# Optimization experiments

Hardware: AMD Instinct MI355X
Metric: run time of the kernel (lower is better)

The kernel has to match this reference:

```python
import jax, jax.numpy as jnp
import numpy as np

D_E = 100   # entity embedding dim
D_R = 100   # relation embedding dim
RANK = 40   # TR rank
N_ENT = 10000
N_REL = 50
B = 128
EPS = 1e-5  # torch BatchNorm1d default eps


def _bn(x, gamma, beta):
    # BatchNorm1d in training mode: biased batch statistics over the batch dim.
    mu = x.mean(axis=0)
    var = x.var(axis=0)  # ddof=0, matches torch normalization variance
    return gamma * (x - mu) * jax.lax.rsqrt(var + EPS) + beta


def _tr_to_tensor(f0, f1, f2, f3):
    # Tensor-ring reconstruction of W with ring trace; factors are [R, d, R].
    # Pairwise contraction keeps intermediates at [R, d, d, R] (256 MB max).
    A = jnp.einsum('aib,bjc->aijc', f0, f1)   # [R, d_r, d_e, R]
    C = jnp.einsum('ckd,dla->ckla', f2, f3)   # [R, d_e, d_e, R]
    return jnp.einsum('aijc,ckla->ijkl', A, C)  # [d_r, d_e, d_e, d_e]


def setup_inputs() -> dict:
    key = jax.random.key(0)
    ks = jax.random.split(key, 10)
    E_weight = 0.001 * jax.random.normal(ks[0], (N_ENT, D_E), dtype=jnp.float32)
    E_weight = E_weight.at[0].set(0.0)  # padding_idx=0
    R_weight = 0.001 * jax.random.normal(ks[1], (N_REL, D_R), dtype=jnp.float32)
    R_weight = R_weight.at[0].set(0.0)
    f0 = jax.random.normal(ks[2], (RANK, D_R, RANK), dtype=jnp.float32) * 0.05
    f1 = jax.random.normal(ks[3], (RANK, D_E, RANK), dtype=jnp.float32) * 0.05
    f2 = jax.random.normal(ks[4], (RANK, D_E, RANK), dtype=jnp.float32) * 0.05
    f3 = jax.random.normal(ks[5], (RANK, D_E, RANK), dtype=jnp.float32) * 0.05
    bnr_g = jnp.ones((D_R,), jnp.float32); bnr_b = jnp.zeros((D_R,), jnp.float32)
    bne_g = jnp.ones((D_E,), jnp.float32); bne_b = jnp.zeros((D_E,), jnp.float32)
    bnw_g = jnp.ones((D_E,), jnp.float32); bnw_b = jnp.zeros((D_E,), jnp.float32)
    r_idx = jax.random.randint(ks[6], (B,), 0, N_REL)
    e_idx1 = jax.random.randint(ks[7], (B,), 0, N_ENT)
    e_idx2 = jax.random.randint(ks[8], (B,), 0, N_ENT)
    return {
        'E_weight': E_weight, 'R_weight': R_weight,
        'f0': f0, 'f1': f1, 'f2': f2, 'f3': f3,
        'bnr_g': bnr_g, 'bnr_b': bnr_b,
        'bne_g': bne_g, 'bne_b': bne_b,
        'bnw_g': bnw_g, 'bnw_b': bnw_b,
        'r_idx': r_idx, 'e_idx1': e_idx1, 'e_idx2': e_idx2,
        'miss_ent_domain': 2,
    }


def reference(E_weight, R_weight, f0, f1, f2, f3,
              bnr_g, bnr_b, bne_g, bne_b, bnw_g, bnw_b,
              r_idx, e_idx1, e_idx2, miss_ent_domain):
    # Reconstruct the full TR tensor every call, as the module does.
    W = _tr_to_tensor(f0, f1, f2, f3)                  # [d_r, d_e, d_e, d_e]
    r = _bn(R_weight[r_idx], bnr_g, bnr_b)             # [B, d_r]
    W_mat = (r @ W.reshape(D_R, -1)).reshape(-1, D_E, D_E, D_E)  # [B, d_e^3]
    # Dropouts are identity here (deterministic / eval mode).
    e1 = _bn(E_weight[e_idx1], bne_g, bne_b)           # [B, d_e]
    e2 = _bn(E_weight[e_idx2], bne_g, bne_b)           # [B, d_e]
    labs = 'ijk'  # ary = 3
    out_lab = labs[miss_ent_domain - 1]
    eq = f'b{labs},' + ','.join(f'b{l}' for l in labs if l != out_lab) + f'->b{out_lab}'
    W_out = jnp.einsum(eq, W_mat, e1, e2)              # [B, d_e]
    W_out = _bn(W_out, bnw_g, bnw_b)
    scores = W_out @ E_weight.T                        # [B, N_ENT]
    pred = jax.nn.softmax(scores, axis=1)
    return (pred, W)
```

## Files before the change

### kernel.cpp

```cpp
#include <hip/hip_runtime.h>
#include <hip/hip_bf16.h>

#define DE 100
#define RK 40
#define NENT 10000
#define BATCH 128
#define KDIM 1600
#define MN 10000
#define PRED_SIZE (BATCH*NENT)

typedef __bf16 bf16x8 __attribute__((ext_vector_type(8)));
typedef float floatx4 __attribute__((ext_vector_type(4)));

static __device__ __forceinline__ unsigned short f2bf(float f) {
    unsigned int u = __builtin_bit_cast(unsigned int, f);
    unsigned int lsb = (u >> 16) & 1u;
    u += 0x7fffu + lsb;
    return (unsigned short)(u >> 16);
}

__global__ void prep_A_kernel(const float* __restrict__ f0, const float* __restrict__ f1,
                              unsigned short* __restrict__ Abf) {
    const int m = blockIdx.x;
    const int i = m / 100, j = m % 100;
    const int t = threadIdx.x;
    __shared__ __align__(16) float P[KDIM];
    __shared__ __align__(16) float Q[KDIM];
    for (int e = t; e < KDIM; e += 256) {
        const int u = e / 40, v = e % 40;
        P[e] = f0[u*4000 + i*40 + v];
        Q[e] = f1[u*4000 + j*40 + v];
    }
    __syncthreads();
    for (int o = t; o < 400; o += 256) {
        const int x  = o / 10;
        const int z4 = (o % 10) * 4;
        float a0=0.f, a1=0.f, a2=0.f, a3=0.f;
        #pragma unroll
        for (int y = 0; y < 40; ++y) {
            const float s = P[x*40 + y];
            const float4 q = *reinterpret_cast<const float4*>(&Q[y*40 + z4]);
            a0 += s*q.x; a1 += s*q.y; a2 += s*q.z; a3 += s*q.w;
        }
        ushort4 r;
        r.x = f2bf(a0); r.y = f2bf(a1); r.z = f2bf(a2); r.w = f2bf(a3);
        *reinterpret_cast<ushort4*>(&Abf[(size_t)m*KDIM + x*40 + z4]) = r;
    }
}

__global__ void prep_B_kernel(const float* __restrict__ f2, const float* __restrict__ f3,
                              unsigned short* __restrict__ Bbf) {
    const int n = blockIdx.x;
    const int k = n / 100, l = n % 100;
    const int t = threadIdx.x;
    __shared__ __align__(16) float P[KDIM];
    __shared__ __align__(16) float Q[KDIM];
    __shared__ __align__(16) float Rt[KDIM];
    for (int e = t; e < KDIM; e += 256) {
        const int u = e / 40, v = e % 40;
        P[e] = f2[u*4000 + k*40 + v];
        Q[e] = f3[u*4000 + l*40 + v];
    }
    __syncthreads();
    for (int o = t; o < 400; o += 256) {
        const int x  = o / 10;
        const int z4 = (o % 10) * 4;
        float a0=0.f, a1=0.f, a2=0.f, a3=0.f;
        #pragma unroll
        for (int y = 0; y < 40; ++y) {
            const float s = P[x*40 + y];
            const float4 q = *reinterpret_cast<const float4*>(&Q[y*40 + z4]);
            a0 += s*q.x; a1 += s*q.y; a2 += s*q.z; a3 += s*q.w;
        }
        Rt[x*40 + z4 + 0] = a0; Rt[x*40 + z4 + 1] = a1;
        Rt[x*40 + z4 + 2] = a2; Rt[x*40 + z4 + 3] = a3;
    }
    __syncthreads();
    for (int o = t; o < 400; o += 256) {
        const int a  = o / 10;
        const int c4 = (o % 10) * 4;
        ushort4 r;
        r.x = f2bf(Rt[(c4+0)*40 + a]);
        r.y = f2bf(Rt[(c4+1)*40 + a]);
        r.z = f2bf(Rt[(c4+2)*40 + a]);
        r.w = f2bf(Rt[(c4+3)*40 + a]);
        *reinterpret_cast<ushort4*>(&Bbf[(size_t)n*KDIM + a*40 + c4]) = r;
    }
}

typedef __attribute__((address_space(1))) void gvoid;
typedef __attribute__((address_space(3))) void lvoid;
static __device__ __forceinline__ void async_cp16(const void* g, void* l) {
    gvoid* gp = (gvoid*)(unsigned long long)g;
    lvoid* lp = (lvoid*)(unsigned int)(unsigned long long)l;
    __builtin_amdgcn_global_load_lds(gp, lp, 16, 0, 0);
}

#define NKT 25
#define LDS_TILE 16384

__global__ __launch_bounds__(512, 2) void gemm_kernel(const unsigned short* __restrict__ A,
                                                      const unsigned short* __restrict__ Bm,
                                                      float* __restrict__ W) {
    extern __shared__ unsigned short lds[];
    const int t = threadIdx.x;
    const int w = t >> 6, l = t & 63;
    const int wm = w >> 2, wn = w & 3;
    const int quad = l >> 4, lrow = l & 15;
    const int swz = lrow & 7;

    const int orig = blockIdx.x;
    const int sb = (orig & 7) * 200 + (orig >> 3);
    const int by = sb / 40, bx = sb % 40;
    const int m0 = by * 256, n0 = bx * 256;

    const int srow = t >> 3;
    const int schk = (t & 7) ^ (srow & 7);
    int offA[4], offB[4];
    #pragma unroll
    for (int i = 0; i < 4; ++i) {
        int ra = m0 + i*64 + srow; if (ra > MN-1) ra = MN-1;
        int rb = n0 + i*64 + srow; if (rb > MN-1) rb = MN-1;
        offA[i] = ra * KDIM + schk * 8;
        offB[i] = rb * KDIM + schk * 8;
    }
    const int lds_off = t * 8;

    floatx4 acc[8][4] = {};

    #pragma unroll
    for (int i = 0; i < 4; ++i) {
        async_cp16(A  + offA[i], lds + i*4096 + lds_off);
        async_cp16(Bm + offB[i], lds + LDS_TILE + i*4096 + lds_off);
    }

    for (int kt = 0; kt < NKT; ++kt) {
        const int cur = kt & 1;
        const unsigned short* As = lds + cur * (2*LDS_TILE);
        const unsigned short* Bs = As + LDS_TILE;

        if (kt < NKT-1) {
            unsigned short* An = lds + (cur ^ 1) * (2*LDS_TILE);
            unsigned short* Bn = An + LDS_TILE;
            const int koff = (kt + 1) * 64;
            #pragma unroll
            for (int i = 0; i < 4; ++i) {
                async_cp16(A  + offA[i] + koff, An + i*4096 + lds_off);
                async_cp16(Bm + offB[i] + koff, Bn + i*4096 + lds_off);
            }
            asm volatile("s_waitcnt vmcnt(8)" ::: "memory");
        } else {
            asm volatile("s_waitcnt vmcnt(0)" ::: "memory");
        }
        __builtin_amdgcn_s_barrier();
        asm volatile("" ::: "memory");

        bf16x8 b[4][2];
        #pragma unroll
        for (int ni = 0; ni < 4; ++ni) {
            const int row = wn*64 + ni*16 + lrow;
            #pragma unroll
            for (int kk = 0; kk < 2; ++kk) {
                const int ch = ((kk << 2) | quad) ^ swz;
                b[ni][kk] = *reinterpret_cast<const bf16x8*>(&Bs[row*64 + ch*8]);
            }
        }
        #pragma unroll
        for (int mh = 0; mh < 2; ++mh) {
            bf16x8 a[4][2];
            #pragma unroll
            for (int mi2 = 0; mi2 < 4; ++mi2) {
                const int row = wm*128 + mh*64 + mi2*16 + lrow;
                #pragma unroll
                for (int kk = 0; kk < 2; ++kk) {
                    const int ch = ((kk << 2) | quad) ^ swz;
                    a[mi2][kk] = *reinterpret_cast<const bf16x8*>(&As[row*64 + ch*8]);
                }
            }
            __builtin_amdgcn_s_setprio(1);
            #pragma unroll
            for (int mi2 = 0; mi2 < 4; ++mi2) {
                #pragma unroll
                for (int ni = 0; ni < 4; ++ni) {
                    acc[mh*4+mi2][ni] = __builtin_amdgcn_mfma_f32_16x16x32_bf16(
                        a[mi2][0], b[ni][0], acc[mh*4+mi2][ni], 0, 0, 0);
                    acc[mh*4+mi2][ni] = __builtin_amdgcn_mfma_f32_16x16x32_bf16(
                        a[mi2][1], b[ni][1], acc[mh*4+mi2][ni], 0, 0, 0);
                }
            }
            __builtin_amdgcn_s_setprio(0);
        }

        asm volatile("s_waitcnt lgkmcnt(0)" ::: "memory");
        __builtin_amdgcn_s_barrier();
        asm volatile("" ::: "memory");
    }

    #pragma unroll
    for (int mi = 0; mi < 8; ++mi) {
        #pragma unroll
        for (int ni = 0; ni < 4; ++ni) {
            #pragma unroll
            for (int reg = 0; reg < 4; ++reg) {
                const int rg = m0 + wm*128 + mi*16 + quad*4 + reg;
                const int cg = n0 + wn*64 + ni*16 + lrow;
                if (rg < MN && cg < MN)
                    W[(size_t)rg * MN + cg] = acc[mi][ni][reg];
            }
        }
    }
}

__global__ void bn_kernel(const float* __restrict__ src, const int* __restrict__ idx,
                          const float* __restrict__ gamma, const float* __restrict__ beta,
                          float* __restrict__ out) {
    const int f = blockIdx.x;
    const int b = threadIdx.x;
    __shared__ float red[BATCH];
    const int row = idx ? idx[b] : b;
    const float x = src[row*DE + f];
    red[b] = x; __syncthreads();
    for (int s = 64; s > 0; s >>= 1) { if (b < s) red[b] += red[b + s]; __syncthreads(); }
    const float mu = red[0] * (1.0f/BATCH);
    __syncthreads();
    const float d = x - mu;
    red[b] = d * d; __syncthreads();
    for (int s = 64; s > 0; s >>= 1) { if (b < s) red[b] += red[b + s]; __syncthreads(); }
    const float var = red[0] * (1.0f/BATCH);
    out[b*DE + f] = gamma[f] * d / sqrtf(var + 1e-5f) + beta[f];
}

__global__ void proj_kernel(const float* __restrict__ rb, const float* __restrict__ e1b,
                            const float* __restrict__ e2b,
                            const float* __restrict__ f0, const float* __restrict__ f1,
                            const float* __restrict__ f2, const float* __restrict__ f3,
                            float* __restrict__ wraw) {
    const int b = blockIdx.x, t = threadIdx.x;
    __shared__ float rv[DE], e1v[DE], e2v[DE];
    __shared__ float R0[KDIM], E1[KDIM], E2[KDIM], T[KDIM], S[KDIM];
    if (t < DE) { rv[t] = rb[b*DE+t]; e1v[t] = e1b[b*DE+t]; e2v[t] = e2b[b*DE+t]; }
    __syncthreads();
    for (int e = t; e < KDIM; e += 256) {
        const int u = e / 40, v = e % 40;
        const int base = u*4000 + v;
        float aR=0.f, aE1=0.f, aE2=0.f;
        for (int p = 0; p < DE; ++p) {
            aR  += rv[p]  * f0[base + p*40];
            aE1 += e1v[p] * f1[base + p*40];
            aE2 += e2v[p] * f3[base + p*40];
        }
        R0[e] = aR; E1[e] = aE1; E2[e] = aE2;
    }
    __syncthreads();
    for (int e = t; e < KDIM; e += 256) {
        const int a = e / 40, c = e % 40;
        float acc = 0.f;
        #pragma unroll
        for (int y = 0; y < 40; ++y) acc += R0[a*40+y] * E1[y*40+c];
        T[e] = acc;
    }
    __syncthreads();
    for (int e = t; e < KDIM; e += 256) {
        const int c = e / 40, d = e % 40;
        float acc = 0.f;
        #pragma unroll
        for (int y = 0; y < 40; ++y) acc += T[y*40+c] * E2[d*40+y];
        S[e] = acc;
    }
    __syncthreads();
    if (t < DE) {
        float acc = 0.f;
        for (int c = 0; c < 40; ++c) {
            #pragma unroll
            for (int d = 0; d < 40; ++d)
                acc += S[c*40+d] * f2[c*4000 + t*40 + d];
        }
        wraw[b*DE + t] = acc;
    }
}

__global__ void scores_kernel(const float* __restrict__ wbn, const float* __restrict__ E,
                              float* __restrict__ scores) {
    const int bx = blockIdx.x;
    const int b = bx >> 3, chunk = bx & 7;
    const int t = threadIdx.x;
    __shared__ __align__(16) float wsh[DE];
    if (t < DE) wsh[t] = wbn[b*DE + t];
    __syncthreads();
    const float4* wv = reinterpret_cast<const float4*>(wsh);
    const int n_end = (chunk + 1) * 1250;
    for (int n = chunk*1250 + t; n < n_end; n += 256) {
        const float4* er = reinterpret_cast<const float4*>(E + (size_t)n * DE);
        float acc = 0.f;
        #pragma unroll
        for (int q = 0; q < 25; ++q) {
            const float4 e4 = er[q], w4 = wv[q];
            acc += e4.x*w4.x + e4.y*w4.y + e4.z*w4.z + e4.w*w4.w;
        }
        scores[(size_t)b*NENT + n] = acc;
    }
}

__global__ void softmax_reduce_kernel(const float* __restrict__ scores,
                                      float* __restrict__ rmax, float* __restrict__ rsum) {
    const int b = blockIdx.x, t = threadIdx.x;
    __shared__ float red[256];
    const float* s = scores + (size_t)b*NENT;
    float m = -1e30f;
    for (int n = t; n < NENT; n += 256) m = fmaxf(m, s[n]);
    red[t] = m; __syncthreads();
    for (int st = 128; st > 0; st >>= 1) { if (t < st) red[t] = fmaxf(red[t], red[t+st]); __syncthreads(); }
    m = red[0]; __syncthreads();
    float sum = 0.f;
    for (int n = t; n < NENT; n += 256) sum += expf(s[n] - m);
    red[t] = sum; __syncthreads();
    for (int st = 128; st > 0; st >>= 1) { if (t < st) red[t] += red[t+st]; __syncthreads(); }
    if (t == 0) { rmax[b] = m; rsum[b] = red[0]; }
}

__global__ void pred_kernel(float* __restrict__ out, const float* __restrict__ rmax,
                            const float* __restrict__ rsum) {
    const int i = blockIdx.x*256 + threadIdx.x;
    const int b = i / NENT;
    out[i] = expf(out[i] - rmax[b]) / rsum[b];
}

extern "C" void kernel_launch(void* const* d_in, const int* in_sizes, int n_in,
                              void* d_out, int out_size, void* d_ws, size_t ws_size,
                              hipStream_t stream) {
    (void)in_sizes; (void)n_in; (void)out_size; (void)ws_size;
    const float* E    = (const float*)d_in[0];
    const float* Rw   = (const float*)d_in[1];
    const float* f0   = (const float*)d_in[2];
    const float* f1   = (const float*)d_in[3];
    const float* f2   = (const float*)d_in[4];
    const float* f3   = (const float*)d_in[5];
    const float* bnrg = (const float*)d_in[6];
    const float* bnrb = (const float*)d_in[7];
    const float* bneg = (const float*)d_in[8];
    const float* bneb = (const float*)d_in[9];
    const float* bnwg = (const float*)d_in[10];
    const float* bnwb = (const float*)d_in[11];
    const int* r_idx  = (const int*)d_in[12];
    const int* e_idx1 = (const int*)d_in[13];
    const int* e_idx2 = (const int*)d_in[14];

    float* out = (float*)d_out;
    float* Wt  = out + PRED_SIZE;

    char* ws = (char*)d_ws;
    unsigned short* Abf = (unsigned short*)ws;
    unsigned short* Bbf = (unsigned short*)(ws + 32000000);
    float* rbn  = (float*)(ws + 64000000);
    float* e1bn = rbn  + BATCH*DE;
    float* e2bn = e1bn + BATCH*DE;
    float* wraw = e2bn + BATCH*DE;
    float* wbn  = wraw + BATCH*DE;
    float* rmax = wbn  + BATCH*DE;
    float* rsum = rmax + BATCH;

    static bool s_attr = false;
    if (!s_attr) {
        hipFuncSetAttribute((const void*)gemm_kernel,
                            hipFuncAttributeMaxDynamicSharedMemorySize, 131072);
        s_attr = true;
    }

    prep_A_kernel<<<MN, 256, 0, stream>>>(f0, f1, Abf);
    prep_B_kernel<<<MN, 256, 0, stream>>>(f2, f3, Bbf);
    gemm_kernel<<<1600, 512, 131072, stream>>>(Abf, Bbf, Wt);

    bn_kernel<<<DE, BATCH, 0, stream>>>(Rw, r_idx, bnrg, bnrb, rbn);
    bn_kernel<<<DE, BATCH, 0, stream>>>(E, e_idx1, bneg, bneb, e1bn);
    bn_kernel<<<DE, BATCH, 0, stream>>>(E, e_idx2, bneg, bneb, e2bn);
    proj_kernel<<<BATCH, 256, 0, stream>>>(rbn, e1bn, e2bn, f0, f1, f2, f3, wraw);
    bn_kernel<<<DE, BATCH, 0, stream>>>(wraw, nullptr, bnwg, bnwb, wbn);
    scores_kernel<<<BATCH*8, 256, 0, stream>>>(wbn, E, out);
    softmax_reduce_kernel<<<BATCH, 256, 0, stream>>>(out, rmax, rsum);
    pred_kernel<<<PRED_SIZE/256, 256, 0, stream>>>(out, rmax, rsum);
}
```

Before: 1.161 ms.

## Interleave GEMM LDS staging with MFMA sub-phases and split projection kernel

The main GEMM loop is restructured into four sub-phases per K tile, each issuing async global-to-LDS copies between LDS fragment reads and MFMA groups, with A and B staged separately. The goal is to hide load latency better and to keep fewer A fragments live in registers. Separately, the three input BatchNorm launches are merged into one kernel. The per-batch projection is split into a parallel stage1 (480 blocks with factors cached in LDS) and a stage2 that does the small contractions, spreading the serial per-batch work across more blocks. Stage1 reuses the Abf workspace region for its output, which is safe only because the GEMM has already finished on the same stream.

```diff
diff --git a/kernel.cpp b/kernel.cpp
--- a/kernel.cpp
+++ b/kernel.cpp
@@ -97,7 +97,6 @@
 }
 
 #define NKT 25
-#define LDS_TILE 16384
 
 __global__ __launch_bounds__(512, 2) void gemm_kernel(const unsigned short* __restrict__ A,
                                                       const unsigned short* __restrict__ Bm,
@@ -116,85 +115,100 @@
 
     const int srow = t >> 3;
     const int schk = (t & 7) ^ (srow & 7);
-    int offA[4], offB[4];
+    const unsigned short* gA[4];
+    const unsigned short* gB[4];
     #pragma unroll
     for (int i = 0; i < 4; ++i) {
         int ra = m0 + i*64 + srow; if (ra > MN-1) ra = MN-1;
         int rb = n0 + i*64 + srow; if (rb > MN-1) rb = MN-1;
-        offA[i] = ra * KDIM + schk * 8;
-        offB[i] = rb * KDIM + schk * 8;
-    }
-    const int lds_off = t * 8;
+        gA[i] = A  + (size_t)ra*KDIM + schk*8;
+        gB[i] = Bm + (size_t)rb*KDIM + schk*8;
+    }
+    const int ldst = t * 8;
+
+    const int ch0  = (quad ^ swz) * 8;
+    const int ch1  = ch0 ^ 32;
+    const int aRow = (wm*128 + lrow) * 64;
+    const int bRow = (wn*64  + lrow) * 64;
+    const unsigned short* pAk0[2] = { lds +         aRow + ch0, lds + 32768 + aRow + ch0 };
+    const unsigned short* pAk1[2] = { lds +         aRow + ch1, lds + 32768 + aRow + ch1 };
+    const unsigned short* pBk0[2] = { lds + 16384 + bRow + ch0, lds + 49152 + bRow + ch0 };
+    const unsigned short* pBk1[2] = { lds + 16384 + bRow + ch1, lds + 49152 + bRow + ch1 };
 
     floatx4 acc[8][4] = {};
-
-    #pragma unroll
-    for (int i = 0; i < 4; ++i) {
-        async_cp16(A  + offA[i], lds + i*4096 + lds_off);
-        async_cp16(Bm + offB[i], lds + LDS_TILE + i*4096 + lds_off);
-    }
-
-    for (int kt = 0; kt < NKT; ++kt) {
-        const int cur = kt & 1;
-        const unsigned short* As = lds + cur * (2*LDS_TILE);
-        const unsigned short* Bs = As + LDS_TILE;
-
-        if (kt < NKT-1) {
-            unsigned short* An = lds + (cur ^ 1) * (2*LDS_TILE);
-            unsigned short* Bn = An + LDS_TILE;
-            const int koff = (kt + 1) * 64;
-            #pragma unroll
-            for (int i = 0; i < 4; ++i) {
-                async_cp16(A  + offA[i] + koff, An + i*4096 + lds_off);
-                async_cp16(Bm + offB[i] + koff, Bn + i*4096 + lds_off);
-            }
-            asm volatile("s_waitcnt vmcnt(8)" ::: "memory");
-        } else {
-            asm volatile("s_waitcnt vmcnt(0)" ::: "memory");
-        }
-        __builtin_amdgcn_s_barrier();
-        asm volatile("" ::: "memory");
-
-        bf16x8 b[4][2];
-        #pragma unroll
-        for (int ni = 0; ni < 4; ++ni) {
-            const int row = wn*64 + ni*16 + lrow;
-            #pragma unroll
-            for (int kk = 0; kk < 2; ++kk) {
-                const int ch = ((kk << 2) | quad) ^ swz;
-                b[ni][kk] = *reinterpret_cast<const bf16x8*>(&Bs[row*64 + ch*8]);
-            }
-        }
-        #pragma unroll
-        for (int mh = 0; mh < 2; ++mh) {
-            bf16x8 a[4][2];
-            #pragma unroll
-            for (int mi2 = 0; mi2 < 4; ++mi2) {
-                const int row = wm*128 + mh*64 + mi2*16 + lrow;
-                #pragma unroll
-                for (int kk = 0; kk < 2; ++kk) {
-                    const int ch = ((kk << 2) | quad) ^ swz;
-                    a[mi2][kk] = *reinterpret_cast<const bf16x8*>(&As[row*64 + ch*8]);
-                }
-            }
-            __builtin_amdgcn_s_setprio(1);
-            #pragma unroll
-            for (int mi2 = 0; mi2 < 4; ++mi2) {
-                #pragma unroll
-                for (int ni = 0; ni < 4; ++ni) {
-                    acc[mh*4+mi2][ni] = __builtin_amdgcn_mfma_f32_16x16x32_bf16(
-                        a[mi2][0], b[ni][0], acc[mh*4+mi2][ni], 0, 0, 0);
-                    acc[mh*4+mi2][ni] = __builtin_amdgcn_mfma_f32_16x16x32_bf16(
-                        a[mi2][1], b[ni][1], acc[mh*4+mi2][ni], 0, 0, 0);
-                }
-            }
-            __builtin_amdgcn_s_setprio(0);
-        }
-
-        asm volatile("s_waitcnt lgkmcnt(0)" ::: "memory");
-        __builtin_amdgcn_s_barrier();
-        asm volatile("" ::: "memory");
-    }
+    bf16x8 bfr[4][2], afr[2][2];
+    int kA = 64, kB = 128;
+
+#define RD_B(c)  do { _Pragma("unroll") for (int ni = 0; ni < 4; ++ni) {              \
+        bfr[ni][0] = *reinterpret_cast<const bf16x8*>(pBk0[c] + ni*1024);             \
+        bfr[ni][1] = *reinterpret_cast<const bf16x8*>(pBk1[c] + ni*1024); } } while(0)
+
+#define RD_A(c,p) do { _Pragma("unroll") for (int j = 0; j < 2; ++j) {                \
+        afr[j][0] = *reinterpret_cast<const bf16x8*>(pAk0[c] + (2*(p)+j)*1024);       \
+        afr[j][1] = *reinterpret_cast<const bf16x8*>(pAk1[c] + (2*(p)+j)*1024); } } while(0)
+
+#define STG_A(c,i0) do { unsigned short* d = lds + (((c)^1)*32768) + (i0)*4096 + ldst; \
+        async_cp16(gA[(i0)]   + kA, d);                                                \
+        async_cp16(gA[(i0)+1] + kA, d + 4096); } while(0)
+
+#define STG_B(c,i0) do { unsigned short* d = lds + ((c)*32768) + 16384 + (i0)*4096 + ldst; \
+        async_cp16(gB[(i0)]   + kB, d);                                                \
+        async_cp16(gB[(i0)+1] + kB, d + 4096); } while(0)
+
+#define BARO() do { __builtin_amdgcn_s_barrier();                                      \
+        asm volatile("s_waitcnt lgkmcnt(0)" ::: "memory");                             \
+        __builtin_amdgcn_sched_barrier(0); } while(0)
+
+#define MM(p) do { __builtin_amdgcn_s_setprio(1);                                      \
+        _Pragma("unroll") for (int j = 0; j < 2; ++j)                                  \
+        _Pragma("unroll") for (int ni = 0; ni < 4; ++ni) {                             \
+            acc[2*(p)+j][ni] = __builtin_amdgcn_mfma_f32_16x16x32_bf16(                \
+                afr[j][0], bfr[ni][0], acc[2*(p)+j][ni], 0, 0, 0);                     \
+            acc[2*(p)+j][ni] = __builtin_amdgcn_mfma_f32_16x16x32_bf16(                \
+                afr[j][1], bfr[ni][1], acc[2*(p)+j][ni], 0, 0, 0); }                   \
+        __builtin_amdgcn_s_setprio(0); } while(0)
+
+#define VMW(n) asm volatile("s_waitcnt vmcnt(" #n ")" ::: "memory")
+
+#define TILE(c, AOK, BOK, VMT) do {                                                    \
+        RD_B(c); RD_A(c,0); if (AOK) { STG_A(c,0); }                                   \
+        BARO(); MM(0); __builtin_amdgcn_s_barrier();                                   \
+        RD_A(c,1); if (AOK) { STG_A(c,2); }                                            \
+        BARO(); MM(1); __builtin_amdgcn_s_barrier();                                   \
+        RD_A(c,2); if (BOK) { STG_B(c,0); }                                            \
+        BARO(); MM(2); __builtin_amdgcn_s_barrier();                                   \
+        RD_A(c,3); if (BOK) { STG_B(c,2); }                                            \
+        BARO(); MM(3);                                                                 \
+        VMT;                                                                           \
+        __builtin_amdgcn_s_barrier();                                                  \
+    } while (0)
+
+    #pragma unroll
+    for (int i = 0; i < 4; ++i) async_cp16(gA[i],      lds +          i*4096 + ldst);
+    #pragma unroll
+    for (int i = 0; i < 4; ++i) async_cp16(gB[i],      lds + 16384 +  i*4096 + ldst);
+    #pragma unroll
+    for (int i = 0; i < 4; ++i) async_cp16(gB[i] + 64, lds + 49152 +  i*4096 + ldst);
+    VMW(4);
+    __builtin_amdgcn_s_barrier();
+
+    for (int it = 0; it < 12; ++it) {
+        TILE(0, true, true, VMW(4));
+        kA += 64; kB += 64;
+        if (it < 11) { TILE(1, true, true,  VMW(4)); }
+        else         { TILE(1, true, false, VMW(0)); }
+        kA += 64; kB += 64;
+    }
+    TILE(0, false, false, ((void)0));
+
+#undef RD_B
+#undef RD_A
+#undef STG_A
+#undef STG_B
+#undef BARO
+#undef MM
+#undef VMW
+#undef TILE
 
     #pragma unroll
     for (int mi = 0; mi < 8; ++mi) {
@@ -211,14 +225,42 @@
     }
 }
 
-__global__ void bn_kernel(const float* __restrict__ src, const int* __restrict__ idx,
+__global__ void bn3_kernel(const float* __restrict__ E, const float* __restrict__ Rw,
+                           const int* __restrict__ r_idx, const int* __restrict__ e_idx1,
+                           const int* __restrict__ e_idx2,
+                           const float* __restrict__ bnrg, const float* __restrict__ bnrb,
+                           const float* __restrict__ bneg, const float* __restrict__ bneb,
+                           float* __restrict__ rbn, float* __restrict__ e1bn,
+                           float* __restrict__ e2bn) {
+    const int grp = blockIdx.x / DE;
+    const int f   = blockIdx.x % DE;
+    const int b   = threadIdx.x;
+    const float* src  = (grp == 0) ? Rw   : E;
+    const int*   idx  = (grp == 0) ? r_idx : (grp == 1 ? e_idx1 : e_idx2);
+    const float* gam  = (grp == 0) ? bnrg : bneg;
+    const float* bet  = (grp == 0) ? bnrb : bneb;
+    float* out        = (grp == 0) ? rbn  : (grp == 1 ? e1bn : e2bn);
+    __shared__ float red[BATCH];
+    const int row = idx[b];
+    const float x = src[row*DE + f];
+    red[b] = x; __syncthreads();
+    for (int s = 64; s > 0; s >>= 1) { if (b < s) red[b] += red[b + s]; __syncthreads(); }
+    const float mu = red[0] * (1.0f/BATCH);
+    __syncthreads();
+    const float d = x - mu;
+    red[b] = d * d; __syncthreads();
+    for (int s = 64; s > 0; s >>= 1) { if (b < s) red[b] += red[b + s]; __syncthreads(); }
+    const float var = red[0] * (1.0f/BATCH);
+    out[b*DE + f] = gam[f] * d / sqrtf(var + 1e-5f) + bet[f];
+}
+
+__global__ void bn_kernel(const float* __restrict__ src,
                           const float* __restrict__ gamma, const float* __restrict__ beta,
                           float* __restrict__ out) {
     const int f = blockIdx.x;
     const int b = threadIdx.x;
     __shared__ float red[BATCH];
-    const int row = idx ? idx[b] : b;
-    const float x = src[row*DE + f];
+    const float x = src[b*DE + f];
     red[b] = x; __syncthreads();
     for (int s = 64; s > 0; s >>= 1) { if (b < s) red[b] += red[b + s]; __syncthreads(); }
     const float mu = red[0] * (1.0f/BATCH);
@@ -230,27 +272,43 @@
     out[b*DE + f] = gamma[f] * d / sqrtf(var + 1e-5f) + beta[f];
 }
 
-__global__ void proj_kernel(const float* __restrict__ rb, const float* __restrict__ e1b,
+__global__ void proj_stage1(const float* __restrict__ rb, const float* __restrict__ e1b,
                             const float* __restrict__ e2b,
                             const float* __restrict__ f0, const float* __restrict__ f1,
-                            const float* __restrict__ f2, const float* __restrict__ f3,
+                            const float* __restrict__ f3,
+                            float* __restrict__ outg) {
+    const int bi = blockIdx.x;
+    const int fi = bi / 160, rest = bi % 160;
+    const int u = rest / 4, b0 = (rest % 4) * 32;
+    const float* vec = (fi == 0) ? rb : (fi == 1 ? e1b : e2b);
+    const float* fac = (fi == 0) ? f0 : (fi == 1 ? f1 : f3);
+    float* og = outg + (size_t)fi * (BATCH*KDIM);
+    __shared__ __align__(16) float F[4000];
+    __shared__ __align__(16) float V[3200];
+    const int t = threadIdx.x;
+    for (int e = t; e < 4000; e += 256) F[e] = fac[u*4000 + e];
+    for (int e = t; e < 3200; e += 256) V[e] = vec[b0*100 + e];
+    __syncthreads();
+    #pragma unroll
+    for (int it = 0; it < 5; ++it) {
+        const int o = t + it*256;
+        const int bb = o / 40, v = o % 40;
+        const float* Vb = &V[bb*100];
+        float acc = 0.f;
+        #pragma unroll 4
+        for (int p = 0; p < 100; ++p) acc += Vb[p] * F[p*40 + v];
+        og[(size_t)(b0+bb)*KDIM + u*40 + v] = acc;
+    }
+}
+
+__global__ void proj_stage2(const float* __restrict__ Rg, const float* __restrict__ f2,
                             float* __restrict__ wraw) {
     const int b = blockIdx.x, t = threadIdx.x;
-    __shared__ float rv[DE], e1v[DE], e2v[DE];
     __shared__ float R0[KDIM], E1[KDIM], E2[KDIM], T[KDIM], S[KDIM];
-    if (t < DE) { rv[t] = rb[b*DE+t]; e1v[t] = e1b[b*DE+t]; e2v[t] = e2b[b*DE+t]; }
-    __syncthreads();
-    for (int e = t; e < KDIM; e += 256) {
-        const int u = e / 40, v = e % 40;
-        const int base = u*4000 + v;
-        float aR=0.f, aE1=0.f, aE2=0.f;
-        for (int p = 0; p < DE; ++p) {
-            aR  += rv[p]  * f0[base + p*40];
-            aE1 += e1v[p] * f1[base + p*40];
-            aE2 += e2v[p] * f3[base + p*40];
-        }
-        R0[e] = aR; E1[e] = aE1; E2[e] = aE2;
-    }
+    const float* R0g = Rg + (size_t)b*KDIM;
+    const float* E1g = Rg + (size_t)BATCH*KDIM   + (size_t)b*KDIM;
+    const float* E2g = Rg + (size_t)2*BATCH*KDIM + (size_t)b*KDIM;
+    for (int e = t; e < KDIM; e += 256) { R0[e] = R0g[e]; E1[e] = E1g[e]; E2[e] = E2g[e]; }
     __syncthreads();
     for (int e = t; e < KDIM; e += 256) {
         const int a = e / 40, c = e % 40;
@@ -358,6 +416,7 @@
     float* wbn  = wraw + BATCH*DE;
     float* rmax = wbn  + BATCH*DE;
     float* rsum = rmax + BATCH;
+    float* Rg = (float*)ws;
 
     static bool s_attr = false;
     if (!s_attr) {
@@ -370,11 +429,11 @@
     prep_B_kernel<<<MN, 256, 0, stream>>>(f2, f3, Bbf);
     gemm_kernel<<<1600, 512, 131072, stream>>>(Abf, Bbf, Wt);
 
-    bn_kernel<<<DE, BATCH, 0, stream>>>(Rw, r_idx, bnrg, bnrb, rbn);
-    bn_kernel<<<DE, BATCH, 0, stream>>>(E, e_idx1, bneg, bneb, e1bn);
-    bn_kernel<<<DE, BATCH, 0, stream>>>(E, e_idx2, bneg, bneb, e2bn);
-    proj_kernel<<<BATCH, 256, 0, stream>>>(rbn, e1bn, e2bn, f0, f1, f2, f3, wraw);
-    bn_kernel<<<DE, BATCH, 0, stream>>>(wraw, nullptr, bnwg, bnwb, wbn);
+    bn3_kernel<<<3*DE, BATCH, 0, stream>>>(E, Rw, r_idx, e_idx1, e_idx2,
+                                           bnrg, bnrb, bneg, bneb, rbn, e1bn, e2bn);
+    proj_stage1<<<480, 256, 0, stream>>>(rbn, e1bn, e2bn, f0, f1, f3, Rg);
+    proj_stage2<<<BATCH, 256, 0, stream>>>(Rg, f2, wraw);
+    bn_kernel<<<DE, BATCH, 0, stream>>>(wraw, bnwg, bnwb, wbn);
     scores_kernel<<<BATCH*8, 256, 0, stream>>>(wbn, E, out);
     softmax_reduce_kernel<<<BATCH, 256, 0, stream>>>(out, rmax, rsum);
     pred_kernel<<<PRED_SIZE/256, 256, 0, stream>>>(out, rmax, rsum);
```

Result: slower. 2.092 ms (+80.2%).
